# Performance work log

Measured on AMD Instinct MI355X. Metric: run time of the kernel, lower is better.

Reference implementation:

```python
import jax, jax.numpy as jnp
import numpy as np

N_NODES = 100000
N_EDGES = 200000
B_GRAPHS = 128
H = 8
DC = 256
DE = 124           # dim_embedding; node features are DE + 4 = 128
DV = 64


def setup_inputs() -> dict:
    key = jax.random.key(0)
    ks = jax.random.split(key, 10)

    def unif(k, shape):
        stdv = 1.0 / np.sqrt(shape[-1])
        return jax.random.uniform(k, shape, jnp.float32, -stdv, stdv)

    x = jax.random.normal(ks[0], (N_NODES, DE + 4), jnp.float32)
    edge_index = jax.random.randint(ks[1], (2, N_EDGES), 0, N_NODES)
    batch = jnp.sort(jax.random.randint(ks[2], (N_NODES,), 0, B_GRAPHS))
    context = jax.random.normal(ks[3], (B_GRAPHS, DC), jnp.float32)
    Wq = unif(ks[4], (H, DC, DV))
    Wk = unif(ks[5], (H, DE + 4, DV))
    Wv = unif(ks[6], (H, DE + 4, DV))
    query_coef = unif(ks[7], (1,))
    Wf = unif(ks[8], (DV, DE))
    return {"x": x, "edge_index": edge_index, "batch": batch, "context": context,
            "Wq": Wq, "Wk": Wk, "Wv": Wv, "query_coef": query_coef, "Wf": Wf}


def reference(x, edge_index, batch, context, Wq, Wk, Wv, query_coef, Wf):
    # edge_index is unused by the original forward.
    n_heads, _, dv = Wq.shape
    n_graphs = context.shape[0]

    query = jnp.einsum('bc,hcv->hbv', context, Wq)       # [H, B, Dv]
    keys = jnp.einsum('ne,hev->hnv', x, Wk)              # [H, N, Dv]
    values = jnp.einsum('ne,hev->hnv', x, Wv)            # [H, N, Dv]

    # original builds u = keys @ query^T [H,N,B] then gathers u[h,n,batch[n]];
    # compute only the gathered per-node score directly (same math).
    q_node = query[:, batch, :]                          # [H, N, Dv]
    u = jnp.sum(keys * q_node, axis=-1) / jnp.sqrt(jnp.asarray(dv, x.dtype))  # [H, N]

    # segment softmax per head over nodes of each graph
    seg_max = jax.vmap(lambda s: jax.ops.segment_max(s, batch, num_segments=n_graphs))(u)
    e = jnp.exp(u - seg_max[:, batch])                   # [H, N]
    seg_sum = jax.vmap(lambda s: jax.ops.segment_sum(s, batch, num_segments=n_graphs))(e)
    a = e / (seg_sum[:, batch] + 1e-16)                  # [H, N]

    v = a[..., None] * values                            # [H, N, Dv]
    agg = jax.vmap(lambda s: jax.ops.segment_sum(s, batch, num_segments=n_graphs))(v)  # [H, B, Dv]

    h = query_coef * query + agg                         # [H, B, Dv]
    h = jnp.einsum('hbv,ve->hbe', h, Wf)                 # [H, B, De]
    return jnp.sum(h, axis=0)                            # [B, De]
```

## Files before the change

kernel.cpp:

```cpp
#include <hip/hip_runtime.h>

#define N_NODES 100000
#define B_GRAPHS 128
#define H_HEADS 8
#define DC 256
#define DF 128
#define DV 64
#define DE 124
#define SPLITS 16
#define GROUPS 8
#define PART_STRIDE (H_HEADS * DF + H_HEADS)


__device__ __forceinline__ float red32(float v) {
  v += __int_as_float(__builtin_amdgcn_update_dpp(0, __float_as_int(v), 0xB1,  0xF, 0xF, true));
  v += __int_as_float(__builtin_amdgcn_update_dpp(0, __float_as_int(v), 0x4E,  0xF, 0xF, true));
  v += __int_as_float(__builtin_amdgcn_update_dpp(0, __float_as_int(v), 0x141, 0xF, 0xF, true));
  v += __int_as_float(__builtin_amdgcn_update_dpp(0, __float_as_int(v), 0x140, 0xF, 0xF, true));
  v += __int_as_float(__builtin_amdgcn_ds_swizzle(__float_as_int(v), 0x401f));
  return v;
}

__global__ __launch_bounds__(256) void k_prep(
    const float* __restrict__ context, const float* __restrict__ Wq,
    const float* __restrict__ Wk, const int* __restrict__ batch,
    float* __restrict__ query_ws, float* __restrict__ kq_ws, int* __restrict__ starts)
{
  const int b = blockIdx.x;
  const int t = threadIdx.x;
  __shared__ float ctxs[DC];
  __shared__ float qs[H_HEADS * DV];
  ctxs[t] = context[b * DC + t];
  if (t == 0) {
    int lo = 0, hi = N_NODES;
    while (lo < hi) { int m = (lo + hi) >> 1; if (batch[m] < b) lo = m + 1; else hi = m; }
    starts[b] = lo;
    if (b == 0) starts[B_GRAPHS] = N_NODES;
  }
  __syncthreads();
  if (t < H_HEADS * DV / 4) {
    const int h = t >> 4, v4 = (t & 15) * 4;
    const float4* wq = reinterpret_cast<const float4*>(Wq + (size_t)h * DC * DV + v4);
    float4 acc = make_float4(0.f, 0.f, 0.f, 0.f);
    for (int c = 0; c < DC; ++c) {
      const float4 w = wq[c * (DV / 4)];
      const float cc = ctxs[c];
      acc.x += cc * w.x; acc.y += cc * w.y; acc.z += cc * w.z; acc.w += cc * w.w;
    }
    *reinterpret_cast<float4*>(qs + h * DV + v4) = acc;
    *reinterpret_cast<float4*>(query_ws + (h * B_GRAPHS + b) * DV + v4) = acc;
  }
  __syncthreads();
  for (int i = t; i < H_HEADS * DF; i += 256) {
    const int h = i >> 7;
    const float4* wk = reinterpret_cast<const float4*>(Wk + (size_t)i * DV);
    const float4* q4 = reinterpret_cast<const float4*>(qs + h * DV);
    float acc = 0.f;
    #pragma unroll
    for (int v4 = 0; v4 < DV / 4; ++v4) {
      const float4 a = wk[v4], q = q4[v4];
      acc += a.x * q.x + a.y * q.y + a.z * q.z + a.w * q.w;
    }
    kq_ws[(h * B_GRAPHS + b) * DF + (i & 127)] = acc * 0.125f;
  }
}

__global__ __launch_bounds__(256) void k_main(
    const float* __restrict__ x, const float* __restrict__ kq_ws,
    const int* __restrict__ starts, float* __restrict__ partials)
{
  const int bid = blockIdx.x;
  const int g = bid >> 4, sp = bid & 15;
  const int t = threadIdx.x;
  const int grp = t >> 5, l32 = t & 31;
  const int s0 = starts[g], s1 = starts[g + 1];
  const int len = s1 - s0;
  const int i0 = s0 + (len * sp) / SPLITS;
  const int i1 = s0 + (len * (sp + 1)) / SPLITS;

  float4 kqr[H_HEADS];
  #pragma unroll
  for (int h = 0; h < H_HEADS; ++h)
    kqr[h] = *reinterpret_cast<const float4*>(kq_ws + (h * B_GRAPHS + g) * DF + 4 * l32);

  float4 s[H_HEADS];
  float l[H_HEADS];
  #pragma unroll
  for (int h = 0; h < H_HEADS; ++h) { s[h] = make_float4(0.f, 0.f, 0.f, 0.f); l[h] = 0.f; }

  int n = i0 + grp;
  float4 a0 = make_float4(0.f, 0.f, 0.f, 0.f);
  float4 a1 = make_float4(0.f, 0.f, 0.f, 0.f);
  if (n < i1)          a0 = *reinterpret_cast<const float4*>(x + (size_t)n * DF + 4 * l32);
  if (n + GROUPS < i1) a1 = *reinterpret_cast<const float4*>(x + (size_t)(n + GROUPS) * DF + 4 * l32);
  while (n < i1) {
    float4 a2 = make_float4(0.f, 0.f, 0.f, 0.f);
    if (n + 2 * GROUPS < i1)
      a2 = *reinterpret_cast<const float4*>(x + (size_t)(n + 2 * GROUPS) * DF + 4 * l32);
    float u[H_HEADS];
    #pragma unroll
    for (int h = 0; h < H_HEADS; ++h)
      u[h] = a0.x * kqr[h].x + a0.y * kqr[h].y + a0.z * kqr[h].z + a0.w * kqr[h].w;
    #pragma unroll
    for (int h = 0; h < H_HEADS; ++h) u[h] = red32(u[h]);
    #pragma unroll
    for (int h = 0; h < H_HEADS; ++h) {
      const float e = __expf(u[h]);
      l[h] += e;
      s[h].x += e * a0.x; s[h].y += e * a0.y; s[h].z += e * a0.z; s[h].w += e * a0.w;
    }
    a0 = a1; a1 = a2; n += GROUPS;
  }

  __shared__ float sbuf[GROUPS][H_HEADS * DF];
  __shared__ float lbuf[GROUPS][H_HEADS];
  #pragma unroll
  for (int h = 0; h < H_HEADS; ++h)
    *reinterpret_cast<float4*>(&sbuf[grp][h * DF + 4 * l32]) = s[h];
  if (l32 == 0) {
    #pragma unroll
    for (int h = 0; h < H_HEADS; ++h) lbuf[grp][h] = l[h];
  }
  __syncthreads();
  float* part = partials + (size_t)bid * PART_STRIDE;
  for (int i = t; i < H_HEADS * DF; i += 256) {
    float acc = 0.f;
    #pragma unroll
    for (int gq = 0; gq < GROUPS; ++gq) acc += sbuf[gq][i];
    part[i] = acc;
  }
  if (t < H_HEADS) {
    float acc = 0.f;
    #pragma unroll
    for (int gq = 0; gq < GROUPS; ++gq) acc += lbuf[gq][t];
    part[H_HEADS * DF + t] = acc;
  }
}

__global__ __launch_bounds__(256) void k_final(
    const float* __restrict__ partials, const float* __restrict__ query_ws,
    const float* __restrict__ Wv, const float* __restrict__ Wf,
    const float* __restrict__ qcoef, float* __restrict__ out)
{
  const int g = blockIdx.x;
  const int t = threadIdx.x;
  __shared__ float w[H_HEADS * DF];
  __shared__ float lg[H_HEADS];
  __shared__ float Gp[4][DV];
  const float* part = partials + (size_t)g * SPLITS * PART_STRIDE;
  if (t < H_HEADS) {
    float acc = 0.f;
    for (int sp = 0; sp < SPLITS; ++sp) acc += part[sp * PART_STRIDE + H_HEADS * DF + t];
    lg[t] = acc;
  }
  __syncthreads();
  for (int i = t; i < H_HEADS * DF; i += 256) {
    float acc = 0.f;
    for (int sp = 0; sp < SPLITS; ++sp) acc += part[sp * PART_STRIDE + i];
    w[i] = acc / (lg[i >> 7] + 1e-16f);
  }
  __syncthreads();
  const float qc = qcoef[0];
  const int v = t & 63, p = t >> 6;
  float acc = qc * (query_ws[((2 * p) * B_GRAPHS + g) * DV + v] +
                    query_ws[((2 * p + 1) * B_GRAPHS + g) * DV + v]);
  #pragma unroll
  for (int hh = 2 * p; hh <= 2 * p + 1; ++hh) {
    const float* wv = Wv + ((size_t)hh * DF) * DV + v;
    const float* wh = w + hh * DF;
    for (int e = 0; e < DF; ++e) acc += wh[e] * wv[(size_t)e * DV];
  }
  Gp[p][v] = acc;
  __syncthreads();
  if (t < DE) {
    float o = 0.f;
    for (int v2 = 0; v2 < DV; ++v2) {
      const float Gv = Gp[0][v2] + Gp[1][v2] + Gp[2][v2] + Gp[3][v2];
      o += Gv * Wf[v2 * DE + t];
    }
    out[g * DE + t] = o;
  }
}

extern "C" void kernel_launch(void* const* d_in, const int* in_sizes, int n_in,
                              void* d_out, int out_size, void* d_ws, size_t ws_size,
                              hipStream_t stream) {
  const float* x       = (const float*)d_in[0];
  const int*   batch   = (const int*)d_in[2];
  const float* context = (const float*)d_in[3];
  const float* Wq      = (const float*)d_in[4];
  const float* Wk      = (const float*)d_in[5];
  const float* Wv      = (const float*)d_in[6];
  const float* qc      = (const float*)d_in[7];
  const float* Wf      = (const float*)d_in[8];
  float* out = (float*)d_out;

  float* ws       = (float*)d_ws;
  float* query_ws = ws;
  float* kq_ws    = ws + 65536;
  float* partials = ws + 196608;
  int*   starts   = (int*)(ws + 196608 + B_GRAPHS * SPLITS * PART_STRIDE);

  hipLaunchKernelGGL(k_prep, dim3(B_GRAPHS), dim3(256), 0, stream,
                     context, Wq, Wk, batch, query_ws, kq_ws, starts);
  hipLaunchKernelGGL(k_main, dim3(B_GRAPHS * SPLITS), dim3(256), 0, stream,
                     x, kq_ws, starts, partials);
  hipLaunchKernelGGL(k_final, dim3(B_GRAPHS), dim3(256), 0, stream,
                     partials, query_ws, Wv, Wf, qc, out);
}
```

Baseline: 147.2 us.

## Fuse prep into main kernel with wave-ballot segment search and fewer splits

Merges the query/key-projection prep kernel into the main streaming kernel. Each block now recomputes its graph's query and Wk·q vectors into shared memory and finds its segment bounds with a 32-way ballot search, which removes one launch and the workspace round trip. Blocks grow to 512 threads and splits drop from 16 to 4, with a two-stage shared reduction of the group partials. The cost is redundant per-split recomputation of the projections, plus fewer and larger blocks (512 total) that may lower latency hiding.

```diff
diff --git a/kernel.cpp b/kernel.cpp
--- a/kernel.cpp
+++ b/kernel.cpp
@@ -7,8 +7,9 @@
 #define DF 128
 #define DV 64
 #define DE 124
-#define SPLITS 16
-#define GROUPS 8
+#define SPLITS 4
+#define THREADS 512
+#define GROUPS 16
 #define PART_STRIDE (H_HEADS * DF + H_HEADS)
 
 
@@ -21,37 +22,56 @@
   return v;
 }
 
-__global__ __launch_bounds__(256) void k_prep(
+__global__ __launch_bounds__(THREADS) void k_mainprep(
+    const float* __restrict__ x, const int* __restrict__ batch,
     const float* __restrict__ context, const float* __restrict__ Wq,
-    const float* __restrict__ Wk, const int* __restrict__ batch,
-    float* __restrict__ query_ws, float* __restrict__ kq_ws, int* __restrict__ starts)
+    const float* __restrict__ Wk,
+    float* __restrict__ query_ws, float* __restrict__ partials)
 {
-  const int b = blockIdx.x;
+  const int bid = blockIdx.x;
+  const int g = bid >> 2, sp = bid & 3;
   const int t = threadIdx.x;
+
   __shared__ float ctxs[DC];
   __shared__ float qs[H_HEADS * DV];
-  ctxs[t] = context[b * DC + t];
-  if (t == 0) {
-    int lo = 0, hi = N_NODES;
-    while (lo < hi) { int m = (lo + hi) >> 1; if (batch[m] < b) lo = m + 1; else hi = m; }
-    starts[b] = lo;
-    if (b == 0) starts[B_GRAPHS] = N_NODES;
-  }
-  __syncthreads();
-  if (t < H_HEADS * DV / 4) {
-    const int h = t >> 4, v4 = (t & 15) * 4;
-    const float4* wq = reinterpret_cast<const float4*>(Wq + (size_t)h * DC * DV + v4);
-    float4 acc = make_float4(0.f, 0.f, 0.f, 0.f);
-    for (int c = 0; c < DC; ++c) {
-      const float4 w = wq[c * (DV / 4)];
-      const float cc = ctxs[c];
-      acc.x += cc * w.x; acc.y += cc * w.y; acc.z += cc * w.z; acc.w += cc * w.w;
-    }
-    *reinterpret_cast<float4*>(qs + h * DV + v4) = acc;
-    *reinterpret_cast<float4*>(query_ws + (h * B_GRAPHS + b) * DV + v4) = acc;
-  }
-  __syncthreads();
-  for (int i = t; i < H_HEADS * DF; i += 256) {
+  __shared__ float kqs[H_HEADS * DF];
+  __shared__ float sbuf[8][H_HEADS * DF];
+  __shared__ float lbuf[GROUPS][H_HEADS];
+  __shared__ int srange[2];
+
+  if (t < DC) ctxs[t] = context[g * DC + t];
+
+  if ((t >> 6) == 7) {
+    const int l = t & 31, half = (t >> 5) & 1;
+    const int target = g + half;
+    int lo = 0, len = N_NODES;
+    while (len > 1) {
+      const int chunk = (len + 31) >> 5;
+      const int idx = lo + l * chunk;
+      const bool lt = (idx < lo + len) && (idx < N_NODES) && (batch[idx] < target);
+      const unsigned long long m = __ballot(lt);
+      const unsigned mh = half ? (unsigned)(m >> 32) : (unsigned)(m & 0xffffffffu);
+      const int k = __popc(mh);
+      if (k == 0) break;
+      lo += (k - 1) * chunk + 1;
+      len = chunk;
+    }
+    if (l == 0) srange[half] = lo;
+  }
+  __syncthreads();
+
+  {
+    const int h = t >> 6, v = t & 63;
+    const float* wq = Wq + (size_t)h * DC * DV + v;
+    float acc = 0.f;
+    #pragma unroll 4
+    for (int c = 0; c < DC; ++c) acc += ctxs[c] * wq[(size_t)c * DV];
+    qs[t] = acc;
+    if (sp == 0) query_ws[(h * B_GRAPHS + g) * DV + v] = acc;
+  }
+  __syncthreads();
+
+  for (int i = t; i < H_HEADS * DF; i += THREADS) {
     const int h = i >> 7;
     const float4* wk = reinterpret_cast<const float4*>(Wk + (size_t)i * DV);
     const float4* q4 = reinterpret_cast<const float4*>(qs + h * DV);
@@ -61,19 +81,12 @@
       const float4 a = wk[v4], q = q4[v4];
       acc += a.x * q.x + a.y * q.y + a.z * q.z + a.w * q.w;
     }
-    kq_ws[(h * B_GRAPHS + b) * DF + (i & 127)] = acc * 0.125f;
-  }
-}
-
-__global__ __launch_bounds__(256) void k_main(
-    const float* __restrict__ x, const float* __restrict__ kq_ws,
-    const int* __restrict__ starts, float* __restrict__ partials)
-{
-  const int bid = blockIdx.x;
-  const int g = bid >> 4, sp = bid & 15;
-  const int t = threadIdx.x;
+    kqs[i] = acc * 0.125f;
+  }
+  __syncthreads();
+
   const int grp = t >> 5, l32 = t & 31;
-  const int s0 = starts[g], s1 = starts[g + 1];
+  const int s0 = srange[0], s1 = srange[1];
   const int len = s1 - s0;
   const int i0 = s0 + (len * sp) / SPLITS;
   const int i1 = s0 + (len * (sp + 1)) / SPLITS;
@@ -81,7 +94,7 @@
   float4 kqr[H_HEADS];
   #pragma unroll
   for (int h = 0; h < H_HEADS; ++h)
-    kqr[h] = *reinterpret_cast<const float4*>(kq_ws + (h * B_GRAPHS + g) * DF + 4 * l32);
+    kqr[h] = *reinterpret_cast<const float4*>(kqs + h * DF + 4 * l32);
 
   float4 s[H_HEADS];
   float l[H_HEADS];
@@ -112,21 +125,35 @@
     a0 = a1; a1 = a2; n += GROUPS;
   }
 
-  __shared__ float sbuf[GROUPS][H_HEADS * DF];
-  __shared__ float lbuf[GROUPS][H_HEADS];
-  #pragma unroll
-  for (int h = 0; h < H_HEADS; ++h)
-    *reinterpret_cast<float4*>(&sbuf[grp][h * DF + 4 * l32]) = s[h];
   if (l32 == 0) {
     #pragma unroll
     for (int h = 0; h < H_HEADS; ++h) lbuf[grp][h] = l[h];
   }
+  if (grp >= 8) {
+    #pragma unroll
+    for (int h = 0; h < H_HEADS; ++h)
+      *reinterpret_cast<float4*>(&sbuf[grp - 8][h * DF + 4 * l32]) = s[h];
+  }
+  __syncthreads();
+  if (grp < 8) {
+    #pragma unroll
+    for (int h = 0; h < H_HEADS; ++h) {
+      const float4 o = *reinterpret_cast<const float4*>(&sbuf[grp][h * DF + 4 * l32]);
+      s[h].x += o.x; s[h].y += o.y; s[h].z += o.z; s[h].w += o.w;
+    }
+  }
+  __syncthreads();
+  if (grp < 8) {
+    #pragma unroll
+    for (int h = 0; h < H_HEADS; ++h)
+      *reinterpret_cast<float4*>(&sbuf[grp][h * DF + 4 * l32]) = s[h];
+  }
   __syncthreads();
   float* part = partials + (size_t)bid * PART_STRIDE;
-  for (int i = t; i < H_HEADS * DF; i += 256) {
-    float acc = 0.f;
-    #pragma unroll
-    for (int gq = 0; gq < GROUPS; ++gq) acc += sbuf[gq][i];
+  for (int i = t; i < H_HEADS * DF; i += THREADS) {
+    float acc = 0.f;
+    #pragma unroll
+    for (int gq = 0; gq < 8; ++gq) acc += sbuf[gq][i];
     part[i] = acc;
   }
   if (t < H_HEADS) {
@@ -150,12 +177,14 @@
   const float* part = partials + (size_t)g * SPLITS * PART_STRIDE;
   if (t < H_HEADS) {
     float acc = 0.f;
+    #pragma unroll
     for (int sp = 0; sp < SPLITS; ++sp) acc += part[sp * PART_STRIDE + H_HEADS * DF + t];
     lg[t] = acc;
   }
   __syncthreads();
   for (int i = t; i < H_HEADS * DF; i += 256) {
     float acc = 0.f;
+    #pragma unroll
     for (int sp = 0; sp < SPLITS; ++sp) acc += part[sp * PART_STRIDE + i];
     w[i] = acc / (lg[i >> 7] + 1e-16f);
   }
@@ -197,14 +226,10 @@
 
   float* ws       = (float*)d_ws;
   float* query_ws = ws;
-  float* kq_ws    = ws + 65536;
-  float* partials = ws + 196608;
-  int*   starts   = (int*)(ws + 196608 + B_GRAPHS * SPLITS * PART_STRIDE);
-
-  hipLaunchKernelGGL(k_prep, dim3(B_GRAPHS), dim3(256), 0, stream,
-                     context, Wq, Wk, batch, query_ws, kq_ws, starts);
-  hipLaunchKernelGGL(k_main, dim3(B_GRAPHS * SPLITS), dim3(256), 0, stream,
-                     x, kq_ws, starts, partials);
+  float* partials = ws + 65536;
+
+  hipLaunchKernelGGL(k_mainprep, dim3(B_GRAPHS * SPLITS), dim3(THREADS), 0, stream,
+                     x, batch, context, Wq, Wk, query_ws, partials);
   hipLaunchKernelGGL(k_final, dim3(B_GRAPHS), dim3(256), 0, stream,
                      partials, query_ws, Wv, Wf, qc, out);
 }
```

New measurement: 153.1 us. +4.0%, slower.
